# Kernel tuning notes

Measured on AMD Instinct MI355X. Metric: run time of the kernel, lower is better.

The kernel has to match this reference:

```python
import jax, jax.numpy as jnp
import numpy as np
import math

GROUPS = 32
HEADS = 8
EPS = 1e-5


def group_norm(x, w, b):
    B, C, H, W = x.shape
    xg = x.reshape(B, GROUPS, C // GROUPS, H, W)
    mu = xg.mean(axis=(2, 3, 4), keepdims=True)
    var = xg.var(axis=(2, 3, 4), keepdims=True)
    xg = (xg - mu) * jax.lax.rsqrt(var + EPS)
    return xg.reshape(B, C, H, W) * w[None, :, None, None] + b[None, :, None, None]


def setup_inputs() -> dict:
    key = jax.random.key(0)
    ks = jax.random.split(key, 3)
    C = 512
    x = jax.random.normal(ks[0], (4, C, 64, 64), dtype=jnp.float32)
    norm_w = jnp.ones((C,), dtype=jnp.float32)
    norm_b = jnp.zeros((C,), dtype=jnp.float32)
    qkv_w = jax.random.normal(ks[1], (3 * C, C), dtype=jnp.float32) * 0.02
    qkv_b = jnp.zeros((3 * C,), dtype=jnp.float32)
    proj_w = jax.random.normal(ks[2], (C, C), dtype=jnp.float32) * 0.02
    proj_b = jnp.zeros((C,), dtype=jnp.float32)
    return {"x": x, "norm_w": norm_w, "norm_b": norm_b, "qkv_w": qkv_w,
            "qkv_b": qkv_b, "proj_w": proj_w, "proj_b": proj_b}


def reference(x, norm_w, norm_b, qkv_w, qkv_b, proj_w, proj_b):
    B, C, H, W = x.shape
    S = H * W
    head_dim = C // HEADS
    scale = 1.0 / math.sqrt(head_dim)

    h = group_norm(x, norm_w, norm_b)
    # 1x1 conv == pointwise linear over channels
    qkv = jnp.einsum('oc,bchw->bohw', qkv_w, h) + qkv_b[None, :, None, None]
    q, k, v = jnp.split(qkv, 3, axis=1)
    q = q.reshape(B, HEADS, head_dim, S)
    k = k.reshape(B, HEADS, head_dim, S)
    v = v.reshape(B, HEADS, head_dim, S)

    # chunked softmax attention in the original is row-wise softmax, i.e.
    # mathematically identical to full attention over all queries
    attn = jnp.einsum('bhdi,bhdj->bhij', q, k) * scale  # [B,H,S,S]
    attn = jax.nn.softmax(attn, axis=-1)
    out = jnp.einsum('bhij,bhdj->bhdi', attn, v)  # [B,H,d,S]

    out = out.reshape(B, C, H, W)
    out = jnp.einsum('oc,bchw->bohw', proj_w, out) + proj_b[None, :, None, None]
    return out + x
```

## Files before the change

kernel.cpp:

```cpp
#include <hip/hip_runtime.h>
#include <hip/hip_bf16.h>

#define NB 4
#define NC 512
#define NS 4096
#define NH 8
#define HD 64
#define NG 32
#define CPG 16
#define QKC 1024
#define CQF 0.18033688f

typedef __attribute__((ext_vector_type(8))) short bf16x8;
typedef __attribute__((ext_vector_type(4))) float f32x4;
typedef __attribute__((ext_vector_type(16))) float f32x16;

__device__ __forceinline__ unsigned short f2bf(float f) {
  union { float f; unsigned int u; } v; v.f = f;
  unsigned int r = v.u + 0x7FFFu + ((v.u >> 16) & 1u);
  return (unsigned short)(r >> 16);
}

__device__ __forceinline__ unsigned short f2bf_rn(float f) {
  union { __hip_bfloat16 h; unsigned short u; } cv;
  cv.h = __float2bfloat16(f);
  return cv.u;
}

__device__ __forceinline__ void gload16(const unsigned short* g, unsigned short* s) {
  __builtin_amdgcn_global_load_lds(
      (const __attribute__((address_space(1))) unsigned int*)g,
      (__attribute__((address_space(3))) unsigned int*)s, 16, 0, 0);
}

__global__ __launch_bounds__(256) void prep_k(const float* __restrict__ x,
                                              float* __restrict__ pstats,
                                              const float* __restrict__ wq,
                                              const float* __restrict__ wp,
                                              unsigned short* __restrict__ wqb,
                                              unsigned short* __restrict__ wpb) {
  int bid = blockIdx.x;
  if (bid < NB * NG * 4) {
    int bgq = bid;
    const float4* xp = (const float4*)(x + (size_t)bgq * (CPG * NS / 4));
    float s = 0.f, s2 = 0.f;
    #pragma unroll 4
    for (int i = threadIdx.x; i < CPG * NS / 16; i += 256) {
      float4 v = xp[i];
      s  += v.x + v.y + v.z + v.w;
      s2 += v.x * v.x + v.y * v.y + v.z * v.z + v.w * v.w;
    }
    #pragma unroll
    for (int off = 32; off > 0; off >>= 1) {
      s  += __shfl_down(s, off);
      s2 += __shfl_down(s2, off);
    }
    __shared__ float rs[4], rs2[4];
    int wid = threadIdx.x >> 6;
    if ((threadIdx.x & 63) == 0) { rs[wid] = s; rs2[wid] = s2; }
    __syncthreads();
    if (threadIdx.x == 0) {
      pstats[bgq * 2]     = rs[0] + rs[1] + rs[2] + rs[3];
      pstats[bgq * 2 + 1] = rs2[0] + rs2[1] + rs2[2] + rs2[3];
    }
  } else {
    const int nq8 = 3 * NC * NC / 8, np8 = NC * NC / 8, se8 = NC * NC / 8;
    int i = (bid - NB * NG * 4) * 256 + threadIdx.x;
    if (i >= nq8 + np8) return;
    const float* src;
    unsigned short* dst;
    float sc;
    int j;
    if (i < nq8) { src = wq; dst = wqb; j = i; sc = (i < se8) ? CQF : 1.0f; }
    else         { src = wp; dst = wpb; j = i - nq8; sc = 1.0f; }
    const float4* s = (const float4*)src + (size_t)j * 2;
    float4 a = s[0], b = s[1];
    ushort4 u0 = make_ushort4(f2bf_rn(a.x * sc), f2bf_rn(a.y * sc),
                              f2bf_rn(a.z * sc), f2bf_rn(a.w * sc));
    ushort4 u1 = make_ushort4(f2bf_rn(b.x * sc), f2bf_rn(b.y * sc),
                              f2bf_rn(b.z * sc), f2bf_rn(b.w * sc));
    uint4 o;
    o.x = (unsigned)u0.x | ((unsigned)u0.y << 16);
    o.y = (unsigned)u0.z | ((unsigned)u0.w << 16);
    o.z = (unsigned)u1.x | ((unsigned)u1.y << 16);
    o.w = (unsigned)u1.z | ((unsigned)u1.w << 16);
    *((uint4*)dst + j) = o;
  }
}

__global__ __launch_bounds__(256) void gn_apply_k(const float* __restrict__ x,
                                                  const float* __restrict__ pstats,
                                                  const float* __restrict__ nw,
                                                  const float* __restrict__ nb,
                                                  unsigned short* __restrict__ ht) {
  int st = blockIdx.x, ct = blockIdx.y, b = blockIdx.z;
  int c0 = ct * 64, s0 = st * 64;
  __shared__ unsigned short lds[64][72];
  for (int idx = threadIdx.x; idx < 1024; idx += 256) {
    int row = idx >> 4, c4 = idx & 15;
    int c = c0 + row;
    int gi = (b * NG + (c >> 4)) * 4;
    const float4* pq = (const float4*)(pstats + gi * 2);
    float4 p01 = pq[0], p23 = pq[1];
    float sum = p01.x + p01.z + p23.x + p23.z;
    float ssq = p01.y + p01.w + p23.y + p23.w;
    float inv_n = 1.0f / (CPG * NS);
    float mu = sum * inv_n;
    float var = ssq * inv_n - mu * mu;
    float rstd = rsqrtf(var + 1e-5f);
    float sw = nw[c] * rstd;
    float sb = nb[c] - mu * sw;
    float4 v = *(const float4*)(x + ((size_t)b * NC + c) * NS + s0 + c4 * 4);
    ushort4 u = make_ushort4(f2bf(v.x * sw + sb), f2bf(v.y * sw + sb),
                             f2bf(v.z * sw + sb), f2bf(v.w * sw + sb));
    *(ushort4*)&lds[row][c4 * 4] = u;
  }
  __syncthreads();
  for (int idx = threadIdx.x; idx < 1024; idx += 256) {
    int i = idx >> 4, ch = idx & 15;
    ushort4 u = make_ushort4(lds[ch * 4 + 0][i], lds[ch * 4 + 1][i],
                             lds[ch * 4 + 2][i], lds[ch * 4 + 3][i]);
    *(ushort4*)(ht + ((size_t)b * NS + s0 + i) * NC + c0 + ch * 4) = u;
  }
}

__global__ __launch_bounds__(256) void qkv_gemm_k(const unsigned short* __restrict__ ht,
                                                  const unsigned short* __restrict__ wqb,
                                                  const float* __restrict__ bq,
                                                  unsigned short* __restrict__ qk,
                                                  unsigned short* __restrict__ vt) {
  int b = blockIdx.z;
  int m0 = blockIdx.x * 128, n0 = blockIdx.y * 128;
  __shared__ unsigned short alds[128 * 64];
  __shared__ unsigned short blds[128 * 64];
  const unsigned short* A = ht + (size_t)b * NS * NC;
  int tid = threadIdx.x;
  int l = tid & 63, w = tid >> 6;
  int wr = w >> 1, wc = w & 1;
  int lm = l & 15, lg = l >> 4;
  int lrow = l >> 3, lcb = l & 7;
  f32x4 acc[4][4];
  #pragma unroll
  for (int mi = 0; mi < 4; mi++)
    #pragma unroll
    for (int ni = 0; ni < 4; ni++) acc[mi][ni] = (f32x4){0.f, 0.f, 0.f, 0.f};

  for (int k0 = 0; k0 < NC; k0 += 64) {
    #pragma unroll
    for (int j = 0; j < 4; j++) {
      int row = w * 32 + j * 8 + lrow;
      int scb = lcb ^ (row & 7);
      gload16(A   + (size_t)(m0 + row) * NC + k0 + scb * 8, &alds[(w * 4 + j) * 512]);
      gload16(wqb + (size_t)(n0 + row) * NC + k0 + scb * 8, &blds[(w * 4 + j) * 512]);
    }
    __syncthreads();
    #pragma unroll
    for (int ks = 0; ks < 2; ks++) {
      bf16x8 af[4], bfr[4];
      #pragma unroll
      for (int mi = 0; mi < 4; mi++) {
        int row = wr * 64 + mi * 16 + lm;
        af[mi] = *(const bf16x8*)&alds[((row << 6) + (ks << 5) + (lg << 3)) ^ ((row & 7) << 3)];
      }
      #pragma unroll
      for (int ni = 0; ni < 4; ni++) {
        int row = wc * 64 + ni * 16 + lm;
        bfr[ni] = *(const bf16x8*)&blds[((row << 6) + (ks << 5) + (lg << 3)) ^ ((row & 7) << 3)];
      }
      #pragma unroll
      for (int mi = 0; mi < 4; mi++)
        #pragma unroll
        for (int ni = 0; ni < 4; ni++)
          acc[mi][ni] = __builtin_amdgcn_mfma_f32_16x16x32_bf16(af[mi], bfr[ni], acc[mi][ni], 0, 0, 0);
    }
    __syncthreads();
  }
  if (n0 < QKC) {
    #pragma unroll
    for (int mi = 0; mi < 4; mi++) {
      #pragma unroll
      for (int ni = 0; ni < 4; ni++) {
        int o = n0 + wc * 64 + ni * 16 + lm;
        float bias = bq[o];
        if (o < NC) bias *= CQF;
        #pragma unroll
        for (int q = 0; q < 4; q++) {
          int s = m0 + wr * 64 + mi * 16 + lg * 4 + q;
          qk[((size_t)b * NS + s) * QKC + o] = f2bf(acc[mi][ni][q] + bias);
        }
      }
    }
  } else {
    #pragma unroll
    for (int mi = 0; mi < 4; mi++) {
      int s0 = m0 + wr * 64 + mi * 16 + lg * 4;
      #pragma unroll
      for (int ni = 0; ni < 4; ni++) {
        int o = n0 + wc * 64 + ni * 16 + lm;
        float bias = bq[o];
        int dg = o - QKC;
        ushort4 u = make_ushort4(f2bf(acc[mi][ni][0] + bias), f2bf(acc[mi][ni][1] + bias),
                                 f2bf(acc[mi][ni][2] + bias), f2bf(acc[mi][ni][3] + bias));
        *(ushort4*)(vt + ((size_t)b * NC + dg) * NS + s0) = u;
      }
    }
  }
}

__global__ __launch_bounds__(512) void attn_k(const unsigned short* __restrict__ qk,
                                              const unsigned short* __restrict__ vt,
                                              unsigned short* __restrict__ ob) {
  int bid = blockIdx.x;
  int xcd = bid & 7, g = bid >> 3;
  int pair = xcd * 4 + (g >> 4);
  int qt = g & 15;
  int h = pair & 7, b = pair >> 3;
  int tid = threadIdx.x;
  int l = tid & 63, w = tid >> 6;
  int l31 = l & 31, hi = l >> 5;
  __shared__ unsigned short slds[16384];
  const unsigned short* qkb = qk + (size_t)b * NS * QKC;
  const unsigned short* vtb = vt + ((size_t)b * NC + h * HD) * NS;
  int iw = qt * 256 + w * 32;

  bf16x8 fq[4];
  #pragma unroll
  for (int kk = 0; kk < 4; kk++)
    fq[kk] = *(const bf16x8*)(qkb + (size_t)(iw + l31) * QKC + h * HD + kk * 16 + hi * 8);

  bf16x8 ones;
  #pragma unroll
  for (int e = 0; e < 8; e++) ones[e] = (short)0x3F80;

  int rb = (((l31 << 6) + (hi << 3)) ^ ((l31 & 7) << 3));
  int rbk[4] = { rb, rb ^ 16, rb ^ 32, rb ^ 48 };

  int kr = w * 8 + (l >> 3);
  int scb = (l & 7) ^ (l >> 3);
  const unsigned short* kgp = qkb + NC + h * HD + (size_t)kr * QKC + scb * 8;
  const unsigned short* vgp = vtb + (size_t)kr * NS + scb * 8;
  unsigned short* kdA = &slds[w * 512];
  unsigned short* kdB = &slds[8192 + w * 512];
  unsigned short* vdA = &slds[4096 + w * 512];
  unsigned short* vdB = &slds[12288 + w * 512];

  f32x16 acc_o0 = {}, acc_o1 = {}, acc_l = {};

  bf16x8 vA[8], vB[8], pA[4], pB[4];
  #pragma unroll
  for (int e = 0; e < 8; e++) vB[e] = (bf16x8){0, 0, 0, 0, 0, 0, 0, 0};
  #pragma unroll
  for (int e = 0; e < 4; e++) pB[e] = (bf16x8){0, 0, 0, 0, 0, 0, 0, 0};

  gload16(kgp, kdA);
  gload16(vgp, vdA);
  kgp += (size_t)64 * QKC; vgp += 64;
  asm volatile("s_waitcnt vmcnt(0)" ::: "memory");
  __syncthreads();

  #define CVTSW(SA, q, DST) {                                                       \
    unsigned X0, X1, Y0, Y1;                                                        \
    asm("v_cvt_pk_bf16_f32 %0, %1, %2" : "=v"(X0) : "v"(SA[q*8+0]), "v"(SA[q*8+1]));\
    asm("v_cvt_pk_bf16_f32 %0, %1, %2" : "=v"(X1) : "v"(SA[q*8+2]), "v"(SA[q*8+3]));\
    asm("v_cvt_pk_bf16_f32 %0, %1, %2" : "=v"(Y0) : "v"(SA[q*8+4]), "v"(SA[q*8+5]));\
    asm("v_cvt_pk_bf16_f32 %0, %1, %2" : "=v"(Y1) : "v"(SA[q*8+6]), "v"(SA[q*8+7]));\
    asm("v_permlane32_swap_b32 %0, %1" : "+v"(X0), "+v"(Y0));                       \
    asm("v_permlane32_swap_b32 %0, %1" : "+v"(X1), "+v"(Y1));                       \
    union { unsigned u[4]; bf16x8 v; } pu = {{X0, X1, Y0, Y1}};                     \
    DST = pu.v; }

  #define TILE(BUF, t, VN, VP, PN, PP, KD, VD) {                                    \
    if ((t) + 1 < 64) {                                                             \
      gload16(kgp, KD);                                                             \
      gload16(vgp, VD);                                                             \
      kgp += (size_t)64 * QKC; vgp += 64;                                           \
    }                                                                               \
    const unsigned short* Kr = &slds[(BUF)*8192];                                   \
    const unsigned short* Vr = &slds[(BUF)*8192 + 4096];                            \
    f32x16 sa0 = {}, sa1 = {};                                                      \
    __builtin_amdgcn_s_setprio(1);                                                  \
    _Pragma("unroll")                                                               \
    for (int kk = 0; kk < 4; kk++) {                                                \
      bf16x8 ak = *(const bf16x8*)&Kr[rbk[kk]];                                     \
      sa0 = __builtin_amdgcn_mfma_f32_32x32x16_bf16(ak, fq[kk], sa0, 0, 0, 0);      \
    }                                                                               \
    _Pragma("unroll")                                                               \
    for (int kk = 0; kk < 4; kk++) {                                                \
      bf16x8 ak = *(const bf16x8*)&Kr[rbk[kk] + 2048];                              \
      sa1 = __builtin_amdgcn_mfma_f32_32x32x16_bf16(ak, fq[kk], sa1, 0, 0, 0);      \
    }                                                                               \
    _Pragma("unroll")                                                               \
    for (int kk = 0; kk < 4; kk++) {                                                \
      VN[kk]     = *(const bf16x8*)&Vr[rbk[kk]];                                    \
      VN[kk + 4] = *(const bf16x8*)&Vr[rbk[kk] + 2048];                             \
    }                                                                               \
    _Pragma("unroll")                                                               \
    for (int bq_ = 0; bq_ < 4; bq_++) {                                             \
      acc_l  = __builtin_amdgcn_mfma_f32_32x32x16_bf16(PP[bq_], ones, acc_l, 0, 0, 0);        \
      acc_o0 = __builtin_amdgcn_mfma_f32_32x32x16_bf16(PP[bq_], VP[bq_], acc_o0, 0, 0, 0);    \
      acc_o1 = __builtin_amdgcn_mfma_f32_32x32x16_bf16(PP[bq_], VP[bq_ + 4], acc_o1, 0, 0, 0);\
    }                                                                               \
    __builtin_amdgcn_s_setprio(0);                                                  \
    _Pragma("unroll")                                                               \
    for (int r = 0; r < 16; r++) {                                                  \
      sa0[r] = __builtin_amdgcn_exp2f(sa0[r]);                                      \
      sa1[r] = __builtin_amdgcn_exp2f(sa1[r]);                                      \
    }                                                                               \
    CVTSW(sa0, 0, PN[0]);                                                           \
    CVTSW(sa0, 1, PN[1]);                                                           \
    CVTSW(sa1, 0, PN[2]);                                                           \
    CVTSW(sa1, 1, PN[3]);                                                           \
    asm volatile("s_waitcnt vmcnt(0)" ::: "memory");                                \
    __syncthreads(); }

  for (int t = 0; t < 64; t += 2) {
    TILE(0, t,     vA, vB, pA, pB, kdB, vdB)
    TILE(1, t + 1, vB, vA, pB, pA, kdA, vdA)
  }
  #undef TILE
  #undef CVTSW

  #pragma unroll
  for (int bq_ = 0; bq_ < 4; bq_++) {
    acc_l  = __builtin_amdgcn_mfma_f32_32x32x16_bf16(pB[bq_], ones, acc_l, 0, 0, 0);
    acc_o0 = __builtin_amdgcn_mfma_f32_32x32x16_bf16(pB[bq_], vB[bq_], acc_o0, 0, 0, 0);
    acc_o1 = __builtin_amdgcn_mfma_f32_32x32x16_bf16(pB[bq_], vB[bq_ + 4], acc_o1, 0, 0, 0);
  }

  #pragma unroll
  for (int r = 0; r < 16; r++) {
    float inv = __builtin_amdgcn_rcpf(acc_l[r]);
    int i = (r & 3) + 8 * (r >> 2) + 4 * hi;
    size_t rowo = ((size_t)b * NS + (iw + i)) * NC + h * HD;
    ob[rowo + l31]      = f2bf_rn(acc_o0[r] * inv);
    ob[rowo + 32 + l31] = f2bf_rn(acc_o1[r] * inv);
  }
}

__global__ __launch_bounds__(256) void proj_gemm_k(const unsigned short* __restrict__ wpb,
                                                   const float* __restrict__ bp,
                                                   const unsigned short* __restrict__ obuf,
                                                   const float* __restrict__ x,
                                                   float* __restrict__ out) {
  int b = blockIdx.z;
  int m0 = blockIdx.x * 128, n0 = blockIdx.y * 128;
  __shared__ unsigned short alds[128 * 64];
  __shared__ unsigned short blds[128 * 64];
  const unsigned short* Bt = obuf + (size_t)b * NS * NC;
  int tid = threadIdx.x;
  int l = tid & 63, w = tid >> 6;
  int wr = w >> 1, wc = w & 1;
  int lm = l & 15, lg = l >> 4;
  int lrow = l >> 3, lcb = l & 7;
  f32x4 acc[4][4];
  #pragma unroll
  for (int mi = 0; mi < 4; mi++)
    #pragma unroll
    for (int ni = 0; ni < 4; ni++) acc[mi][ni] = (f32x4){0.f, 0.f, 0.f, 0.f};

  for (int k0 = 0; k0 < NC; k0 += 64) {
    #pragma unroll
    for (int j = 0; j < 4; j++) {
      int row = w * 32 + j * 8 + lrow;
      int scb = lcb ^ (row & 7);
      gload16(wpb + (size_t)(m0 + row) * NC + k0 + scb * 8, &alds[(w * 4 + j) * 512]);
      gload16(Bt  + (size_t)(n0 + row) * NC + k0 + scb * 8, &blds[(w * 4 + j) * 512]);
    }
    __syncthreads();
    #pragma unroll
    for (int ks = 0; ks < 2; ks++) {
      bf16x8 af[4], bfr[4];
      #pragma unroll
      for (int mi = 0; mi < 4; mi++) {
        int row = wr * 64 + mi * 16 + lm;
        af[mi] = *(const bf16x8*)&alds[((row << 6) + (ks << 5) + (lg << 3)) ^ ((row & 7) << 3)];
      }
      #pragma unroll
      for (int ni = 0; ni < 4; ni++) {
        int row = wc * 64 + ni * 16 + lm;
        bfr[ni] = *(const bf16x8*)&blds[((row << 6) + (ks << 5) + (lg << 3)) ^ ((row & 7) << 3)];
      }
      #pragma unroll
      for (int mi = 0; mi < 4; mi++)
        #pragma unroll
        for (int ni = 0; ni < 4; ni++)
          acc[mi][ni] = __builtin_amdgcn_mfma_f32_16x16x32_bf16(af[mi], bfr[ni], acc[mi][ni], 0, 0, 0);
    }
    __syncthreads();
  }
  #pragma unroll
  for (int mi = 0; mi < 4; mi++) {
    #pragma unroll
    for (int q = 0; q < 4; q++) {
      int o = m0 + wr * 64 + mi * 16 + lg * 4 + q;
      float bias = bp[o];
      #pragma unroll
      for (int ni = 0; ni < 4; ni++) {
        int s = n0 + wc * 64 + ni * 16 + lm;
        size_t idx = ((size_t)b * NC + o) * NS + s;
        out[idx] = acc[mi][ni][q] + bias + x[idx];
      }
    }
  }
}

extern "C" void kernel_launch(void* const* d_in, const int* in_sizes, int n_in,
                              void* d_out, int out_size, void* d_ws, size_t ws_size,
                              hipStream_t stream) {
  const float* x  = (const float*)d_in[0];
  const float* nw = (const float*)d_in[1];
  const float* nb = (const float*)d_in[2];
  const float* wq = (const float*)d_in[3];
  const float* bq = (const float*)d_in[4];
  const float* wp = (const float*)d_in[5];
  const float* bp = (const float*)d_in[6];
  float* out = (float*)d_out;

  char* ws = (char*)d_ws;
  size_t off = 0;
  off += 1024;
  unsigned short* ht  = (unsigned short*)(ws + off); off += (size_t)NB * NS * NC * 2;
  unsigned short* qk  = (unsigned short*)(ws + off); off += (size_t)NB * NS * QKC * 2;
  unsigned short* vt  = (unsigned short*)(ws + off); off += (size_t)NB * NS * NC * 2;
  unsigned short* wqb = (unsigned short*)(ws + off); off += (size_t)3 * NC * NC * 2;
  unsigned short* wpb = (unsigned short*)(ws + off); off += (size_t)NC * NC * 2;
  unsigned short* ob  = ht;
  float* pstats = (float*)qk;

  prep_k<<<dim3(1024), 256, 0, stream>>>(x, pstats, wq, wp, wqb, wpb);
  gn_apply_k<<<dim3(NS / 64, NC / 64, NB), 256, 0, stream>>>(x, pstats, nw, nb, ht);
  qkv_gemm_k<<<dim3(NS / 128, 1536 / 128, NB), 256, 0, stream>>>(ht, wqb, bq, qk, vt);
  attn_k<<<dim3(512), 512, 0, stream>>>(qk, vt, ob);
  proj_gemm_k<<<dim3(NC / 128, NS / 128, NB), 256, 0, stream>>>(wpb, bp, ob, x, out);
}
```

Measured before the change: 219.6 us.

## Triple-buffer K/V tiles in attention kernel with partial vmcnt waits

```diff
diff --git a/kernel.cpp b/kernel.cpp
--- a/kernel.cpp
+++ b/kernel.cpp
@@ -218,7 +218,7 @@
   int tid = threadIdx.x;
   int l = tid & 63, w = tid >> 6;
   int l31 = l & 31, hi = l >> 5;
-  __shared__ unsigned short slds[16384];
+  __shared__ unsigned short slds[24576];
   const unsigned short* qkb = qk + (size_t)b * NS * QKC;
   const unsigned short* vtb = vt + ((size_t)b * NC + h * HD) * NS;
   int iw = qt * 256 + w * 32;
@@ -239,10 +239,12 @@
   int scb = (l & 7) ^ (l >> 3);
   const unsigned short* kgp = qkb + NC + h * HD + (size_t)kr * QKC + scb * 8;
   const unsigned short* vgp = vtb + (size_t)kr * NS + scb * 8;
-  unsigned short* kdA = &slds[w * 512];
-  unsigned short* kdB = &slds[8192 + w * 512];
-  unsigned short* vdA = &slds[4096 + w * 512];
-  unsigned short* vdB = &slds[12288 + w * 512];
+  unsigned short* kd0 = &slds[w * 512];
+  unsigned short* kd1 = kd0 + 8192;
+  unsigned short* kd2 = kd0 + 16384;
+  unsigned short* vd0 = &slds[4096 + w * 512];
+  unsigned short* vd1 = vd0 + 8192;
+  unsigned short* vd2 = vd0 + 16384;
 
   f32x16 acc_o0 = {}, acc_o1 = {}, acc_l = {};
 
@@ -252,11 +254,12 @@
   #pragma unroll
   for (int e = 0; e < 4; e++) pB[e] = (bf16x8){0, 0, 0, 0, 0, 0, 0, 0};
 
-  gload16(kgp, kdA);
-  gload16(vgp, vdA);
+  gload16(kgp, kd0); gload16(vgp, vd0);
   kgp += (size_t)64 * QKC; vgp += 64;
-  asm volatile("s_waitcnt vmcnt(0)" ::: "memory");
-  __syncthreads();
+  gload16(kgp, kd1); gload16(vgp, vd1);
+  kgp += (size_t)64 * QKC; vgp += 64;
+  asm volatile("s_waitcnt vmcnt(2)" ::: "memory");
+  __builtin_amdgcn_s_barrier();
 
   #define CVTSW(SA, q, DST) {                                                       \
     unsigned X0, X1, Y0, Y1;                                                        \
@@ -269,14 +272,13 @@
     union { unsigned u[4]; bf16x8 v; } pu = {{X0, X1, Y0, Y1}};                     \
     DST = pu.v; }
 
-  #define TILE(BUF, t, VN, VP, PN, PP, KD, VD) {                                    \
-    if ((t) + 1 < 64) {                                                             \
-      gload16(kgp, KD);                                                             \
-      gload16(vgp, VD);                                                             \
+  #define TILE(RB, IB, WC, VN, VP, PN, PP) {                                        \
+    if (WC) {                                                                       \
+      gload16(kgp, kd##IB); gload16(vgp, vd##IB);                                   \
       kgp += (size_t)64 * QKC; vgp += 64;                                           \
     }                                                                               \
-    const unsigned short* Kr = &slds[(BUF)*8192];                                   \
-    const unsigned short* Vr = &slds[(BUF)*8192 + 4096];                            \
+    const unsigned short* Kr = &slds[(RB)*8192];                                    \
+    const unsigned short* Vr = &slds[(RB)*8192 + 4096];                             \
     f32x16 sa0 = {}, sa1 = {};                                                      \
     __builtin_amdgcn_s_setprio(1);                                                  \
     _Pragma("unroll")                                                               \
@@ -310,13 +312,22 @@
     CVTSW(sa0, 1, PN[1]);                                                           \
     CVTSW(sa1, 0, PN[2]);                                                           \
     CVTSW(sa1, 1, PN[3]);                                                           \
-    asm volatile("s_waitcnt vmcnt(0)" ::: "memory");                                \
-    __syncthreads(); }
-
-  for (int t = 0; t < 64; t += 2) {
-    TILE(0, t,     vA, vB, pA, pB, kdB, vdB)
-    TILE(1, t + 1, vB, vA, pB, pA, kdA, vdA)
-  }
+    if (WC) asm volatile("s_waitcnt vmcnt(2) lgkmcnt(0)" ::: "memory");             \
+    else    asm volatile("s_waitcnt vmcnt(0) lgkmcnt(0)" ::: "memory");             \
+    __builtin_amdgcn_s_barrier(); }
+
+  for (int it = 0; it < 10; ++it) {
+    TILE(0, 2, 2, vA, vB, pA, pB)
+    TILE(1, 0, 2, vB, vA, pB, pA)
+    TILE(2, 1, 2, vA, vB, pA, pB)
+    TILE(0, 2, 2, vB, vA, pB, pA)
+    TILE(1, 0, 2, vA, vB, pA, pB)
+    TILE(2, 1, 2, vB, vA, pB, pA)
+  }
+  TILE(0, 2, 2, vA, vB, pA, pB)
+  TILE(1, 0, 2, vB, vA, pB, pA)
+  TILE(2, 0, 0, vA, vB, pA, pB)
+  TILE(0, 0, 0, vB, vA, pB, pA)
   #undef TILE
   #undef CVTSW
 
```

After: 220.5 us. No clear change (+0.4%).

## Process two KV tiles per barrier round with doubled LDS staging

Applied to the files above, without the earlier changes.

```diff
diff --git a/kernel.cpp b/kernel.cpp
--- a/kernel.cpp
+++ b/kernel.cpp
@@ -218,7 +218,7 @@
   int tid = threadIdx.x;
   int l = tid & 63, w = tid >> 6;
   int l31 = l & 31, hi = l >> 5;
-  __shared__ unsigned short slds[16384];
+  __shared__ unsigned short slds[32768];
   const unsigned short* qkb = qk + (size_t)b * NS * QKC;
   const unsigned short* vtb = vt + ((size_t)b * NC + h * HD) * NS;
   int iw = qt * 256 + w * 32;
@@ -239,22 +239,16 @@
   int scb = (l & 7) ^ (l >> 3);
   const unsigned short* kgp = qkb + NC + h * HD + (size_t)kr * QKC + scb * 8;
   const unsigned short* vgp = vtb + (size_t)kr * NS + scb * 8;
-  unsigned short* kdA = &slds[w * 512];
-  unsigned short* kdB = &slds[8192 + w * 512];
-  unsigned short* vdA = &slds[4096 + w * 512];
-  unsigned short* vdB = &slds[12288 + w * 512];
+  unsigned short* kd = &slds[w * 512];
+  unsigned short* vd = &slds[4096 + w * 512];
 
   f32x16 acc_o0 = {}, acc_o1 = {}, acc_l = {};
 
-  bf16x8 vA[8], vB[8], pA[4], pB[4];
-  #pragma unroll
-  for (int e = 0; e < 8; e++) vB[e] = (bf16x8){0, 0, 0, 0, 0, 0, 0, 0};
-  #pragma unroll
-  for (int e = 0; e < 4; e++) pB[e] = (bf16x8){0, 0, 0, 0, 0, 0, 0, 0};
-
-  gload16(kgp, kdA);
-  gload16(vgp, vdA);
-  kgp += (size_t)64 * QKC; vgp += 64;
+  gload16(kgp, kd);
+  gload16(kgp + (size_t)64 * QKC, kd + 8192);
+  gload16(vgp, vd);
+  gload16(vgp + 64, vd + 8192);
+  kgp += (size_t)128 * QKC; vgp += 128;
   asm volatile("s_waitcnt vmcnt(0)" ::: "memory");
   __syncthreads();
 
@@ -269,63 +263,91 @@
     union { unsigned u[4]; bf16x8 v; } pu = {{X0, X1, Y0, Y1}};                     \
     DST = pu.v; }
 
-  #define TILE(BUF, t, VN, VP, PN, PP, KD, VD) {                                    \
-    if ((t) + 1 < 64) {                                                             \
-      gload16(kgp, KD);                                                             \
-      gload16(vgp, VD);                                                             \
-      kgp += (size_t)64 * QKC; vgp += 64;                                           \
-    }                                                                               \
-    const unsigned short* Kr = &slds[(BUF)*8192];                                   \
-    const unsigned short* Vr = &slds[(BUF)*8192 + 4096];                            \
-    f32x16 sa0 = {}, sa1 = {};                                                      \
-    __builtin_amdgcn_s_setprio(1);                                                  \
-    _Pragma("unroll")                                                               \
-    for (int kk = 0; kk < 4; kk++) {                                                \
-      bf16x8 ak = *(const bf16x8*)&Kr[rbk[kk]];                                     \
-      sa0 = __builtin_amdgcn_mfma_f32_32x32x16_bf16(ak, fq[kk], sa0, 0, 0, 0);      \
-    }                                                                               \
-    _Pragma("unroll")                                                               \
-    for (int kk = 0; kk < 4; kk++) {                                                \
-      bf16x8 ak = *(const bf16x8*)&Kr[rbk[kk] + 2048];                              \
-      sa1 = __builtin_amdgcn_mfma_f32_32x32x16_bf16(ak, fq[kk], sa1, 0, 0, 0);      \
-    }                                                                               \
-    _Pragma("unroll")                                                               \
-    for (int kk = 0; kk < 4; kk++) {                                                \
-      VN[kk]     = *(const bf16x8*)&Vr[rbk[kk]];                                    \
-      VN[kk + 4] = *(const bf16x8*)&Vr[rbk[kk] + 2048];                             \
-    }                                                                               \
-    _Pragma("unroll")                                                               \
-    for (int bq_ = 0; bq_ < 4; bq_++) {                                             \
-      acc_l  = __builtin_amdgcn_mfma_f32_32x32x16_bf16(PP[bq_], ones, acc_l, 0, 0, 0);        \
-      acc_o0 = __builtin_amdgcn_mfma_f32_32x32x16_bf16(PP[bq_], VP[bq_], acc_o0, 0, 0, 0);    \
-      acc_o1 = __builtin_amdgcn_mfma_f32_32x32x16_bf16(PP[bq_], VP[bq_ + 4], acc_o1, 0, 0, 0);\
-    }                                                                               \
-    __builtin_amdgcn_s_setprio(0);                                                  \
-    _Pragma("unroll")                                                               \
-    for (int r = 0; r < 16; r++) {                                                  \
-      sa0[r] = __builtin_amdgcn_exp2f(sa0[r]);                                      \
-      sa1[r] = __builtin_amdgcn_exp2f(sa1[r]);                                      \
-    }                                                                               \
-    CVTSW(sa0, 0, PN[0]);                                                           \
-    CVTSW(sa0, 1, PN[1]);                                                           \
-    CVTSW(sa1, 0, PN[2]);                                                           \
-    CVTSW(sa1, 1, PN[3]);                                                           \
-    asm volatile("s_waitcnt vmcnt(0)" ::: "memory");                                \
-    __syncthreads(); }
-
-  for (int t = 0; t < 64; t += 2) {
-    TILE(0, t,     vA, vB, pA, pB, kdB, vdB)
-    TILE(1, t + 1, vB, vA, pB, pA, kdA, vdA)
-  }
-  #undef TILE
+  #define SUB_QK(KRBASE, SA0, SA1) {                                               \
+    const unsigned short* Kr = (KRBASE);                                           \
+    _Pragma("unroll")                                                              \
+    for (int kk = 0; kk < 4; kk++) {                                               \
+      bf16x8 ak = *(const bf16x8*)&Kr[rbk[kk]];                                    \
+      SA0 = __builtin_amdgcn_mfma_f32_32x32x16_bf16(ak, fq[kk], SA0, 0, 0, 0);     \
+    }                                                                              \
+    _Pragma("unroll")                                                              \
+    for (int kk = 0; kk < 4; kk++) {                                               \
+      bf16x8 ak = *(const bf16x8*)&Kr[rbk[kk] + 2048];                             \
+      SA1 = __builtin_amdgcn_mfma_f32_32x32x16_bf16(ak, fq[kk], SA1, 0, 0, 0);     \
+    }}
+
+  #define SUB_SMPV(SA0, SA1, VRBASE) {                                             \
+    _Pragma("unroll")                                                              \
+    for (int r = 0; r < 16; r++) {                                                 \
+      SA0[r] = __builtin_amdgcn_exp2f(SA0[r]);                                     \
+      SA1[r] = __builtin_amdgcn_exp2f(SA1[r]);                                     \
+    }                                                                              \
+    bf16x8 p0_, p1_, p2_, p3_;                                                     \
+    CVTSW(SA0, 0, p0_);                                                            \
+    CVTSW(SA0, 1, p1_);                                                            \
+    CVTSW(SA1, 0, p2_);                                                            \
+    CVTSW(SA1, 1, p3_);                                                            \
+    const unsigned short* Vr = (VRBASE);                                           \
+    __builtin_amdgcn_s_setprio(1);                                                 \
+    {                                                                              \
+      bf16x8 bv0 = *(const bf16x8*)&Vr[rbk[0]];                                    \
+      bf16x8 bv1 = *(const bf16x8*)&Vr[rbk[0] + 2048];                             \
+      acc_l  = __builtin_amdgcn_mfma_f32_32x32x16_bf16(p0_, ones, acc_l, 0, 0, 0); \
+      acc_o0 = __builtin_amdgcn_mfma_f32_32x32x16_bf16(p0_, bv0, acc_o0, 0, 0, 0); \
+      acc_o1 = __builtin_amdgcn_mfma_f32_32x32x16_bf16(p0_, bv1, acc_o1, 0, 0, 0); \
+    }                                                                              \
+    {                                                                              \
+      bf16x8 bv0 = *(const bf16x8*)&Vr[rbk[1]];                                    \
+      bf16x8 bv1 = *(const bf16x8*)&Vr[rbk[1] + 2048];                             \
+      acc_l  = __builtin_amdgcn_mfma_f32_32x32x16_bf16(p1_, ones, acc_l, 0, 0, 0); \
+      acc_o0 = __builtin_amdgcn_mfma_f32_32x32x16_bf16(p1_, bv0, acc_o0, 0, 0, 0); \
+      acc_o1 = __builtin_amdgcn_mfma_f32_32x32x16_bf16(p1_, bv1, acc_o1, 0, 0, 0); \
+    }                                                                              \
+    {                                                                              \
+      bf16x8 bv0 = *(const bf16x8*)&Vr[rbk[2]];                                    \
+      bf16x8 bv1 = *(const bf16x8*)&Vr[rbk[2] + 2048];                             \
+      acc_l  = __builtin_amdgcn_mfma_f32_32x32x16_bf16(p2_, ones, acc_l, 0, 0, 0); \
+      acc_o0 = __builtin_amdgcn_mfma_f32_32x32x16_bf16(p2_, bv0, acc_o0, 0, 0, 0); \
+      acc_o1 = __builtin_amdgcn_mfma_f32_32x32x16_bf16(p2_, bv1, acc_o1, 0, 0, 0); \
+    }                                                                              \
+    {                                                                              \
+      bf16x8 bv0 = *(const bf16x8*)&Vr[rbk[3]];                                    \
+      bf16x8 bv1 = *(const bf16x8*)&Vr[rbk[3] + 2048];                             \
+      acc_l  = __builtin_amdgcn_mfma_f32_32x32x16_bf16(p3_, ones, acc_l, 0, 0, 0); \
+      acc_o0 = __builtin_amdgcn_mfma_f32_32x32x16_bf16(p3_, bv0, acc_o0, 0, 0, 0); \
+      acc_o1 = __builtin_amdgcn_mfma_f32_32x32x16_bf16(p3_, bv1, acc_o1, 0, 0, 0); \
+    }                                                                              \
+    __builtin_amdgcn_s_setprio(0); }
+
+  #define ROUND(BUF, t) {                                                          \
+    if ((t) + 1 < 32) {                                                            \
+      unsigned short* kdn = &slds[((BUF) ^ 1) * 16384 + w * 512];                  \
+      unsigned short* vdn = kdn + 4096;                                            \
+      gload16(kgp, kdn);                                                           \
+      gload16(kgp + (size_t)64 * QKC, kdn + 8192);                                 \
+      gload16(vgp, vdn);                                                           \
+      gload16(vgp + 64, vdn + 8192);                                               \
+      kgp += (size_t)128 * QKC; vgp += 128;                                        \
+    }                                                                              \
+    const unsigned short* base = &slds[(BUF) * 16384];                             \
+    f32x16 sa0 = {}, sa1 = {}, sb0 = {}, sb1 = {};                                 \
+    __builtin_amdgcn_s_setprio(1);                                                 \
+    SUB_QK(base, sa0, sa1)                                                         \
+    SUB_QK(base + 8192, sb0, sb1)                                                  \
+    __builtin_amdgcn_s_setprio(0);                                                 \
+    SUB_SMPV(sa0, sa1, base + 4096)                                                \
+    SUB_SMPV(sb0, sb1, base + 12288)                                               \
+    asm volatile("s_waitcnt vmcnt(0) lgkmcnt(0)" ::: "memory");                    \
+    __builtin_amdgcn_s_barrier(); }
+
+  for (int t = 0; t < 32; t += 2) {
+    ROUND(0, t)
+    ROUND(1, t + 1)
+  }
+  #undef ROUND
+  #undef SUB_SMPV
+  #undef SUB_QK
   #undef CVTSW
-
-  #pragma unroll
-  for (int bq_ = 0; bq_ < 4; bq_++) {
-    acc_l  = __builtin_amdgcn_mfma_f32_32x32x16_bf16(pB[bq_], ones, acc_l, 0, 0, 0);
-    acc_o0 = __builtin_amdgcn_mfma_f32_32x32x16_bf16(pB[bq_], vB[bq_], acc_o0, 0, 0, 0);
-    acc_o1 = __builtin_amdgcn_mfma_f32_32x32x16_bf16(pB[bq_], vB[bq_ + 4], acc_o1, 0, 0, 0);
-  }
 
   #pragma unroll
   for (int r = 0; r < 16; r++) {
```

New measurement: 217.1 us, median of 2. About the same (-1.1%).
